# Performance work log

Hardware: AMD Instinct MI355X
Metric: run time of the kernel (lower is better)

Reference implementation:

```python
import jax, jax.numpy as jnp
import numpy as np

D_MODEL = 256
N = 8192

def setup_inputs() -> dict:
    key = jax.random.key(0)
    k1, k2, k3, k4 = jax.random.split(key, 4)
    x = jax.random.normal(k1, (N, D_MODEL), dtype=jnp.float32)
    # nn.Linear weights: shape [out, in], applied as x @ W.T
    s = 1.0 / np.sqrt(D_MODEL)
    Wq = jax.random.normal(k2, (D_MODEL, D_MODEL), dtype=jnp.float32) * s
    Wk = jax.random.normal(k3, (D_MODEL, D_MODEL), dtype=jnp.float32) * s
    Wv = jax.random.normal(k4, (D_MODEL, D_MODEL), dtype=jnp.float32) * s
    return {"x": x, "Wq": Wq, "Wk": Wk, "Wv": Wv}

def reference(x, Wq, Wk, Wv):
    d_model = Wq.shape[0]
    Q = x @ Wq.T  # [N, d]
    K = x @ Wk.T
    V = x @ Wv.T
    scores = (Q @ K.T) / jnp.sqrt(jnp.asarray(d_model, x.dtype))  # [N, N]
    attn = jax.nn.softmax(scores, axis=-1)  # stable max-sub softmax, same math
    cntx = attn @ V  # [N, d]
    return (cntx, attn)
```

## Files before the change

### kernel.cpp

```cpp
#include <hip/hip_runtime.h>

#define D_MODEL 256
#define NSEQ    8192
#define PV_GROUPS 4

typedef _Float16 half8 __attribute__((ext_vector_type(8)));
typedef _Float16 half4 __attribute__((ext_vector_type(4)));
typedef float    f32x4 __attribute__((ext_vector_type(4)));

__device__ __forceinline__ half8 cvt8(f32x4 a, f32x4 b) {
  half8 h;
  h[0]=(_Float16)a[0]; h[1]=(_Float16)a[1]; h[2]=(_Float16)a[2]; h[3]=(_Float16)a[3];
  h[4]=(_Float16)b[0]; h[5]=(_Float16)b[1]; h[6]=(_Float16)b[2]; h[7]=(_Float16)b[3];
  return h;
}

__device__ __forceinline__ half8 load8_f32(const float* p) {
  f32x4 a = *(const f32x4*)p;
  f32x4 b = *(const f32x4*)(p + 4);
  return cvt8(a, b);
}

__global__ __launch_bounds__(256) void qkv_kernel(
    const float* __restrict__ x, const float* __restrict__ Wq,
    const float* __restrict__ Wk, const float* __restrict__ Wv,
    _Float16* __restrict__ QK16, _Float16* __restrict__ VT)
{
  const int tid  = threadIdx.x;
  const int lane = tid & 63;
  const int wave = tid >> 6;
  const int c    = lane & 15;
  const int quad = lane >> 4;
  const int M0   = blockIdx.x * 128 + (wave >> 1) * 64;
  const int Nblk = blockIdx.y * 128 + (wave & 1) * 64;
  const int widx = Nblk >> 8;
  const int nloc = Nblk & 255;
  const float* W = (widx == 0) ? Wq : (widx == 1 ? Wk : Wv);

  f32x4 acc[4][4] = {};
  for (int k0 = 0; k0 < D_MODEL; k0 += 32) {
    half8 af[4], bf[4];
#pragma unroll
    for (int mt = 0; mt < 4; ++mt)
      af[mt] = load8_f32(&x[(size_t)(M0 + mt*16 + c) * D_MODEL + k0 + quad*8]);
#pragma unroll
    for (int nt = 0; nt < 4; ++nt)
      bf[nt] = load8_f32(&W[(size_t)(nloc + nt*16 + c) * D_MODEL + k0 + quad*8]);
#pragma unroll
    for (int mt = 0; mt < 4; ++mt)
#pragma unroll
      for (int nt = 0; nt < 4; ++nt)
        acc[mt][nt] = __builtin_amdgcn_mfma_f32_16x16x32_f16(af[mt], bf[nt], acc[mt][nt], 0, 0, 0);
  }

  if (widx < 2) {
#pragma unroll
    for (int mt = 0; mt < 4; ++mt)
#pragma unroll
      for (int nt = 0; nt < 4; ++nt) {
        const int col  = widx * 256 + nloc + nt*16 + c;
        const int row0 = M0 + mt*16 + quad*4;
#pragma unroll
        for (int r = 0; r < 4; ++r)
          QK16[(size_t)(row0 + r) * 512 + col] = (_Float16)acc[mt][nt][r];
      }
  } else {
#pragma unroll
    for (int mt = 0; mt < 4; ++mt)
#pragma unroll
      for (int nt = 0; nt < 4; ++nt) {
        const int d  = nloc + nt*16 + c;
        const int m0 = M0 + mt*16 + quad*4;
        half4 h;
        h[0]=(_Float16)acc[mt][nt][0]; h[1]=(_Float16)acc[mt][nt][1];
        h[2]=(_Float16)acc[mt][nt][2]; h[3]=(_Float16)acc[mt][nt][3];
        *(half4*)&VT[(size_t)d * NSEQ + m0] = h;
      }
  }
}

__global__ __launch_bounds__(256) void score_kernel(
    const _Float16* __restrict__ QK16, float* __restrict__ S,
    float* __restrict__ lsum)
{
  const int tid  = threadIdx.x;
  const int lane = tid & 63;
  const int wave = tid >> 6;
  const int c    = lane & 15;
  const int quad = lane >> 4;
  const int M0   = blockIdx.x * 128 + (wave >> 1) * 64;
  const int N0   = blockIdx.y * 128 + (wave & 1) * 64;

  f32x4 acc[4][4] = {};
  for (int k0 = 0; k0 < 256; k0 += 32) {
    half8 af[4], bf[4];
#pragma unroll
    for (int mt = 0; mt < 4; ++mt)
      af[mt] = *(const half8*)&QK16[(size_t)(M0 + mt*16 + c) * 512 + k0 + quad*8];
#pragma unroll
    for (int nt = 0; nt < 4; ++nt)
      bf[nt] = *(const half8*)&QK16[(size_t)(N0 + nt*16 + c) * 512 + 256 + k0 + quad*8];
#pragma unroll
    for (int mt = 0; mt < 4; ++mt)
#pragma unroll
      for (int nt = 0; nt < 4; ++nt)
        acc[mt][nt] = __builtin_amdgcn_mfma_f32_16x16x32_f16(af[mt], bf[nt], acc[mt][nt], 0, 0, 0);
  }

  float psum[4][4] = {};
#pragma unroll
  for (int mt = 0; mt < 4; ++mt)
#pragma unroll
    for (int nt = 0; nt < 4; ++nt)
#pragma unroll
      for (int r = 0; r < 4; ++r) {
        const float p = __expf(acc[mt][nt][r] * 0.0625f);
        psum[mt][r] += p;
        S[(size_t)(M0 + mt*16 + quad*4 + r) * NSEQ + N0 + nt*16 + c] = p;
      }

#pragma unroll
  for (int mt = 0; mt < 4; ++mt)
#pragma unroll
    for (int r = 0; r < 4; ++r) {
      float v = psum[mt][r];
      v += __shfl_xor(v, 1);
      v += __shfl_xor(v, 2);
      v += __shfl_xor(v, 4);
      v += __shfl_xor(v, 8);
      if (c == 0) atomicAdd(&lsum[M0 + mt*16 + quad*4 + r], v);
    }
}

__global__ __launch_bounds__(256) void pv_kernel(
    float* __restrict__ attn, const float* __restrict__ lsum,
    const _Float16* __restrict__ VT, float* __restrict__ cntx)
{
  __shared__ _Float16 As[64 * 40];
  __shared__ float linv[64];
  const int tid  = threadIdx.x;
  const int lane = tid & 63;
  const int wave = tid >> 6;
  const int c    = lane & 15;
  const int quad = lane >> 4;
  const int M0   = blockIdx.x * 64;
  const int jb   = blockIdx.y * (NSEQ / PV_GROUPS);
  const int je   = jb + NSEQ / PV_GROUPS;
  const int D0   = wave * 64;
  const int sr   = tid >> 2;
  const int sc   = (tid & 3) * 8;

  if (tid < 64) linv[tid] = 1.0f / lsum[M0 + tid];
  __syncthreads();

  f32x4 acc[4][4] = {};
  for (int j0 = jb; j0 < je; j0 += 32) {
    float* prow = &attn[(size_t)(M0 + sr) * NSEQ + j0 + sc];
    f32x4 p0 = *(f32x4*)prow;
    f32x4 p1 = *(f32x4*)(prow + 4);
    const float s = linv[sr];
    p0 = p0 * s;
    p1 = p1 * s;
    *(f32x4*)prow       = p0;
    *(f32x4*)(prow + 4) = p1;
    __syncthreads();
    *(half8*)&As[sr * 40 + sc] = cvt8(p0, p1);
    __syncthreads();

    half8 af[4], bf[4];
#pragma unroll
    for (int mt = 0; mt < 4; ++mt)
      af[mt] = *(const half8*)&As[(mt*16 + c) * 40 + quad*8];
#pragma unroll
    for (int nt = 0; nt < 4; ++nt)
      bf[nt] = *(const half8*)&VT[(size_t)(D0 + nt*16 + c) * NSEQ + j0 + quad*8];
#pragma unroll
    for (int mt = 0; mt < 4; ++mt)
#pragma unroll
      for (int nt = 0; nt < 4; ++nt)
        acc[mt][nt] = __builtin_amdgcn_mfma_f32_16x16x32_f16(af[mt], bf[nt], acc[mt][nt], 0, 0, 0);
  }

#pragma unroll
  for (int mt = 0; mt < 4; ++mt)
#pragma unroll
    for (int nt = 0; nt < 4; ++nt)
#pragma unroll
      for (int r = 0; r < 4; ++r)
        atomicAdd(&cntx[(size_t)(M0 + mt*16 + quad*4 + r) * D_MODEL + D0 + nt*16 + c],
                  acc[mt][nt][r]);
}

extern "C" void kernel_launch(void* const* d_in, const int* in_sizes, int n_in,
                              void* d_out, int out_size, void* d_ws, size_t ws_size,
                              hipStream_t stream)
{
  const float* x  = (const float*)d_in[0];
  const float* Wq = (const float*)d_in[1];
  const float* Wk = (const float*)d_in[2];
  const float* Wv = (const float*)d_in[3];

  float* cntx = (float*)d_out;
  float* attn = cntx + (size_t)NSEQ * D_MODEL;

  _Float16* QK16 = (_Float16*)d_ws;
  _Float16* VT   = QK16 + (size_t)NSEQ * 512;
  float*    lsum = (float*)(VT + (size_t)D_MODEL * NSEQ);

  hipMemsetAsync(cntx, 0, sizeof(float) * (size_t)NSEQ * D_MODEL, stream);
  hipMemsetAsync(lsum, 0, sizeof(float) * NSEQ, stream);

  qkv_kernel<<<dim3(64, 6), 256, 0, stream>>>(x, Wq, Wk, Wv, QK16, VT);
  score_kernel<<<dim3(64, 64), 256, 0, stream>>>(QK16, attn, lsum);
  pv_kernel<<<dim3(128, PV_GROUPS), 256, 0, stream>>>(attn, lsum, VT, cntx);
}
```

Measured before the change: 604.7 us.

## Stage unnormalized probabilities in fp16 workspace and restructure PV kernel

When the workspace is large enough, the score kernel writes unnormalized exp values as fp16 to scratch rather than fp32 into attn. The PV kernel then reads that fp16 buffer, writes the normalized fp32 attn once, and feeds MFMA directly from global memory instead of staging through LDS. Normalization of the context is moved to the epilogue, and the PV tiling changes to 32 rows by 64 columns with 8 split groups. The aim is to cut the fp32 read-modify-write traffic on the large NxN matrix, at the cost of fp16 rounding of P before normalization and more atomic adds into cntx.

```diff
diff --git a/kernel.cpp b/kernel.cpp
--- a/kernel.cpp
+++ b/kernel.cpp
@@ -2,7 +2,7 @@
 
 #define D_MODEL 256
 #define NSEQ    8192
-#define PV_GROUPS 4
+#define PV_GROUPS 8
 
 typedef _Float16 half8 __attribute__((ext_vector_type(8)));
 typedef _Float16 half4 __attribute__((ext_vector_type(4)));
@@ -79,8 +79,9 @@
   }
 }
 
+template<bool P16>
 __global__ __launch_bounds__(256) void score_kernel(
-    const _Float16* __restrict__ QK16, float* __restrict__ S,
+    const _Float16* __restrict__ QK16, void* __restrict__ Pout,
     float* __restrict__ lsum)
 {
   const int tid  = threadIdx.x;
@@ -116,7 +117,9 @@
       for (int r = 0; r < 4; ++r) {
         const float p = __expf(acc[mt][nt][r] * 0.0625f);
         psum[mt][r] += p;
-        S[(size_t)(M0 + mt*16 + quad*4 + r) * NSEQ + N0 + nt*16 + c] = p;
+        const size_t idx = (size_t)(M0 + mt*16 + quad*4 + r) * NSEQ + N0 + nt*16 + c;
+        if constexpr (P16) ((_Float16*)Pout)[idx] = (_Float16)p;
+        else               ((float*)Pout)[idx]    = p;
       }
 
 #pragma unroll
@@ -132,63 +135,95 @@
     }
 }
 
+template<bool P16>
 __global__ __launch_bounds__(256) void pv_kernel(
-    float* __restrict__ attn, const float* __restrict__ lsum,
-    const _Float16* __restrict__ VT, float* __restrict__ cntx)
-{
-  __shared__ _Float16 As[64 * 40];
-  __shared__ float linv[64];
+    const void* __restrict__ Pin, float* __restrict__ attn,
+    const float* __restrict__ lsum, const _Float16* __restrict__ VT,
+    float* __restrict__ cntx)
+{
+  __shared__ float linv[32];
   const int tid  = threadIdx.x;
   const int lane = tid & 63;
   const int wave = tid >> 6;
   const int c    = lane & 15;
   const int quad = lane >> 4;
-  const int M0   = blockIdx.x * 64;
+  const int M0   = blockIdx.x * 32;
   const int jb   = blockIdx.y * (NSEQ / PV_GROUPS);
   const int je   = jb + NSEQ / PV_GROUPS;
   const int D0   = wave * 64;
-  const int sr   = tid >> 2;
-  const int sc   = (tid & 3) * 8;
-
-  if (tid < 64) linv[tid] = 1.0f / lsum[M0 + tid];
+  const int nr   = tid >> 3;
+  const int ncol = (tid & 7) * 8;
+
+  if (tid < 32) linv[tid] = 1.0f / lsum[M0 + tid];
   __syncthreads();
-
-  f32x4 acc[4][4] = {};
-  for (int j0 = jb; j0 < je; j0 += 32) {
-    float* prow = &attn[(size_t)(M0 + sr) * NSEQ + j0 + sc];
-    f32x4 p0 = *(f32x4*)prow;
-    f32x4 p1 = *(f32x4*)(prow + 4);
-    const float s = linv[sr];
-    p0 = p0 * s;
-    p1 = p1 * s;
-    *(f32x4*)prow       = p0;
-    *(f32x4*)(prow + 4) = p1;
-    __syncthreads();
-    *(half8*)&As[sr * 40 + sc] = cvt8(p0, p1);
-    __syncthreads();
-
-    half8 af[4], bf[4];
-#pragma unroll
-    for (int mt = 0; mt < 4; ++mt)
-      af[mt] = *(const half8*)&As[(mt*16 + c) * 40 + quad*8];
-#pragma unroll
-    for (int nt = 0; nt < 4; ++nt)
-      bf[nt] = *(const half8*)&VT[(size_t)(D0 + nt*16 + c) * NSEQ + j0 + quad*8];
-#pragma unroll
-    for (int mt = 0; mt < 4; ++mt)
-#pragma unroll
-      for (int nt = 0; nt < 4; ++nt)
-        acc[mt][nt] = __builtin_amdgcn_mfma_f32_16x16x32_f16(af[mt], bf[nt], acc[mt][nt], 0, 0, 0);
-  }
-
-#pragma unroll
-  for (int mt = 0; mt < 4; ++mt)
-#pragma unroll
-    for (int nt = 0; nt < 4; ++nt)
-#pragma unroll
-      for (int r = 0; r < 4; ++r)
+  const float nscale = linv[nr];
+
+  f32x4 acc[2][4] = {};
+  for (int j0 = jb; j0 < je; j0 += 64) {
+    half8 np16; f32x4 np0, np1;
+    if constexpr (P16) {
+      np16 = *(const half8*)((const _Float16*)Pin + (size_t)(M0 + nr) * NSEQ + j0 + ncol);
+    } else {
+      const float* pr = (const float*)Pin + (size_t)(M0 + nr) * NSEQ + j0 + ncol;
+      np0 = *(const f32x4*)pr; np1 = *(const f32x4*)(pr + 4);
+    }
+
+    half8 af[2][2], bf[4][2];
+#pragma unroll
+    for (int h = 0; h < 2; ++h) {
+#pragma unroll
+      for (int mt = 0; mt < 2; ++mt) {
+        if constexpr (P16) {
+          af[mt][h] = *(const half8*)((const _Float16*)Pin +
+                        (size_t)(M0 + mt*16 + c) * NSEQ + j0 + h*32 + quad*8);
+        } else {
+          const float* pa = (const float*)Pin +
+                        (size_t)(M0 + mt*16 + c) * NSEQ + j0 + h*32 + quad*8;
+          af[mt][h] = cvt8(*(const f32x4*)pa, *(const f32x4*)(pa + 4));
+        }
+      }
+#pragma unroll
+      for (int nt = 0; nt < 4; ++nt)
+        bf[nt][h] = *(const half8*)&VT[(size_t)(D0 + nt*16 + c) * NSEQ + j0 + h*32 + quad*8];
+    }
+
+    if constexpr (!P16) __syncthreads();
+
+    {
+      float* ar = attn + (size_t)(M0 + nr) * NSEQ + j0 + ncol;
+      f32x4 w0, w1;
+      if constexpr (P16) {
+#pragma unroll
+        for (int r = 0; r < 4; ++r) {
+          w0[r] = (float)np16[r]     * nscale;
+          w1[r] = (float)np16[r + 4] * nscale;
+        }
+      } else {
+        w0 = np0 * nscale; w1 = np1 * nscale;
+      }
+      *(f32x4*)ar       = w0;
+      *(f32x4*)(ar + 4) = w1;
+    }
+
+#pragma unroll
+    for (int h = 0; h < 2; ++h)
+#pragma unroll
+      for (int mt = 0; mt < 2; ++mt)
+#pragma unroll
+        for (int nt = 0; nt < 4; ++nt)
+          acc[mt][nt] = __builtin_amdgcn_mfma_f32_16x16x32_f16(af[mt][h], bf[nt][h], acc[mt][nt], 0, 0, 0);
+  }
+
+#pragma unroll
+  for (int mt = 0; mt < 2; ++mt)
+#pragma unroll
+    for (int r = 0; r < 4; ++r) {
+      const float s = linv[mt*16 + quad*4 + r];
+#pragma unroll
+      for (int nt = 0; nt < 4; ++nt)
         atomicAdd(&cntx[(size_t)(M0 + mt*16 + quad*4 + r) * D_MODEL + D0 + nt*16 + c],
-                  acc[mt][nt][r]);
+                  acc[mt][nt][r] * s);
+    }
 }
 
 extern "C" void kernel_launch(void* const* d_in, const int* in_sizes, int n_in,
@@ -206,11 +241,23 @@
   _Float16* QK16 = (_Float16*)d_ws;
   _Float16* VT   = QK16 + (size_t)NSEQ * 512;
   float*    lsum = (float*)(VT + (size_t)D_MODEL * NSEQ);
+  _Float16* P16  = (_Float16*)(lsum + NSEQ);
+
+  const size_t base_bytes = (size_t)NSEQ*512*2 + (size_t)D_MODEL*NSEQ*2 + (size_t)NSEQ*4;
+  const bool big_ws = ws_size >= base_bytes + (size_t)NSEQ * NSEQ * 2;
 
   hipMemsetAsync(cntx, 0, sizeof(float) * (size_t)NSEQ * D_MODEL, stream);
   hipMemsetAsync(lsum, 0, sizeof(float) * NSEQ, stream);
 
   qkv_kernel<<<dim3(64, 6), 256, 0, stream>>>(x, Wq, Wk, Wv, QK16, VT);
-  score_kernel<<<dim3(64, 64), 256, 0, stream>>>(QK16, attn, lsum);
-  pv_kernel<<<dim3(128, PV_GROUPS), 256, 0, stream>>>(attn, lsum, VT, cntx);
-}
+
+  if (big_ws) {
+    score_kernel<true><<<dim3(64, 64), 256, 0, stream>>>(QK16, (void*)P16, lsum);
+    pv_kernel<true><<<dim3(NSEQ/32, PV_GROUPS), 256, 0, stream>>>(
+        (const void*)P16, attn, lsum, VT, cntx);
+  } else {
+    score_kernel<false><<<dim3(64, 64), 256, 0, stream>>>(QK16, (void*)attn, lsum);
+    pv_kernel<false><<<dim3(NSEQ/32, PV_GROUPS), 256, 0, stream>>>(
+        (const void*)attn, attn, lsum, VT, cntx);
+  }
+}
```

Measured after the change: 656.4 us. 1.09x slower.
